# Optimization experiments

Measured on AMD Instinct MI355X. Metric: run time of the kernel, lower is better.

Reference implementation:

```python
import jax, jax.numpy as jnp
import numpy as np

MESH_SIZE = 0.01
HIDDEN = 256
NUM_LAYERS = 3
TEMP = 1e-3          # soft-relay temperature (forward default)
H_SCALE = 0.0        # soft-magnet: mu0*H << B
M_SCALE = 0.5
M_OFFSET = 0.5


def _make_mesh():
    # Uniform triangular Preisach mesh: points (beta, alpha) with 0 <= beta <= alpha <= 1.
    k = int(round(1.0 / MESH_SIZE)) + 1  # 101 grid lines -> 5151 points
    g = np.linspace(0.0, 1.0, k, dtype=np.float32)
    bb, aa = np.meshgrid(g, g, indexing='ij')
    sel = bb <= aa
    return jnp.asarray(np.stack([bb[sel], aa[sel]], axis=-1))  # [N, 2] = (beta, alpha)


def setup_inputs() -> dict:
    key = jax.random.key(0)
    ks = jax.random.split(key, 10)
    mesh = _make_mesh()                       # [N, 2]
    n = mesh.shape[0]
    B, CTXT, T = 8, 128, 2048
    encoder_input = jax.random.uniform(ks[0], (B, CTXT, 2), dtype=jnp.float32)
    decoder_input = jax.random.uniform(ks[1], (B, T, 1), dtype=jnp.float32)
    initial_states = 2.0 * jax.random.uniform(ks[2], (B, n), dtype=jnp.float32) - 1.0  # s in [-1, 1]
    y0 = jax.random.uniform(ks[3], (B,), dtype=jnp.float32)
    # ResNetMLP density network params (input_dim=2, output_dim=1)
    W_in = jax.random.normal(ks[4], (2, HIDDEN), dtype=jnp.float32) * 0.5
    b_in = jnp.zeros((HIDDEN,), dtype=jnp.float32)
    W_blk = jax.random.normal(ks[5], (NUM_LAYERS, HIDDEN, HIDDEN), dtype=jnp.float32) * (1.0 / np.sqrt(HIDDEN))
    b_blk = jnp.zeros((NUM_LAYERS, HIDDEN), dtype=jnp.float32)
    W_out = jax.random.normal(ks[6], (HIDDEN, 1), dtype=jnp.float32) * (1.0 / np.sqrt(HIDDEN))
    b_out = jnp.zeros((1,), dtype=jnp.float32)
    return {'encoder_input': encoder_input, 'decoder_input': decoder_input,
            'initial_states': initial_states, 'y0': y0, 'mesh': mesh,
            'W_in': W_in, 'b_in': b_in, 'W_blk': W_blk, 'b_blk': b_blk,
            'W_out': W_out, 'b_out': b_out}


def _density(mesh, W_in, b_in, W_blk, b_blk, W_out, b_out):
    # ResNetMLP (eval: dropout off) + sigmoid (normalized_density=True)
    h = jax.nn.relu(mesh @ W_in + b_in)
    for i in range(NUM_LAYERS):  # small fixed layer loop
        h = h + jax.nn.relu(h @ W_blk[i] + b_blk[i])
    return jax.nn.sigmoid((h @ W_out + b_out)[..., 0])  # [N]


def _get_states(h_seq, alpha, beta, s0, h0):
    # Sequential soft-relay hysteron update across time.
    # h_seq [B,T], alpha/beta [N], s0 [B,N], h0 [B]
    def step(carry, h_t):  # h_t [B]
        s, h_prev = carry
        up = jax.nn.sigmoid((h_t[:, None] - alpha[None, :]) / TEMP)   # switch to +1 when h > alpha
        dn = jax.nn.sigmoid((h_t[:, None] - beta[None, :]) / TEMP)    # stay/unswitch vs beta when sweeping down
        s_up = s + (1.0 - s) * up            # increasing field branch
        s_dn = -1.0 + (s + 1.0) * dn         # decreasing field branch
        inc = (h_t >= h_prev)[:, None]
        s_new = jnp.where(inc, s_up, s_dn)
        return (s_new, h_t), s_new
    (_, _), states = jax.lax.scan(step, (s0, h0), jnp.swapaxes(h_seq, 0, 1))
    return jnp.swapaxes(states, 0, 1)  # [B, T, N]


def reference(encoder_input, decoder_input, initial_states, y0, mesh,
              W_in, b_in, W_blk, b_blk, W_out, b_out):
    B = encoder_input.shape[0]
    n = mesh.shape[0]
    beta = mesh[:, 0]
    alpha = mesh[:, 1]
    density = _density(mesh, W_in, b_in, W_blk, b_blk, W_out, b_out)  # [N] (shared mesh, eval)
    h = decoder_input[..., 0]                                          # [B, T]
    states = _get_states(h, alpha, beta, initial_states, y0)           # [B, T, N]
    m = jnp.einsum('n,btn->bt', density, states) / jnp.sum(density)    # [B, T]
    b_norm = H_SCALE * h + M_SCALE * m + M_OFFSET
    density_b = jnp.broadcast_to(density, (B, n))
    mesh_b = jnp.broadcast_to(mesh, (B,) + mesh.shape)
    return (b_norm, density_b, m, initial_states, mesh_b)
```

## Files before the change

kernel.cpp:

```cpp
#include <hip/hip_runtime.h>
#include <hip/hip_fp16.h>
#include <math.h>

#define N_MESH   5151
#define NB       8
#define TT       2048
#define HID      256
#define NLAYERS  3
#define NCHUNK   64
#define CHUNK    32
#define NG       101
#define TROW     40
#define NQ       11
#define NPAD     5632
#define SCAN_GRID 512
#define PREP_NBLK 48
#define COPY_NBLK 61
#define MLP_NBLK  81
#define PH2_NBLK  88
#define DENSB_NBLK 21

#define OFF_SGV   144
#define OFF_TAB   272
#define SMEM1     8352
#define OFF_RED   8352
#define OFF_DRED  12960
#define SMEM3     13088

#define WS_DENSITY 0
#define WS_WT      6144
#define WS_PQ      104448

#define OUT_BNORM  0
#define OUT_DENSB  16384
#define OUT_M      57592
#define OUT_S0     73976
#define OUT_MESHB  115184

typedef _Float16 half8  __attribute__((ext_vector_type(8)));
typedef unsigned short u16x8 __attribute__((ext_vector_type(8)));
typedef float    f32x4  __attribute__((ext_vector_type(4)));

__device__ __forceinline__ float sigmoid_fast(float x) {
    float e = __expf(-x);
    return __builtin_amdgcn_rcpf(1.0f + e);
}

__device__ __forceinline__ int swz(int row, int kbyte) {
    return row * 512 + (kbyte ^ ((row & 7) << 4));
}

__device__ __forceinline__ float dpp16_sum(float v) {
    int a;
    a = __builtin_amdgcn_update_dpp(0, __float_as_int(v), 0xB1, 0xF, 0xF, true);
    v += __int_as_float(a);
    a = __builtin_amdgcn_update_dpp(0, __float_as_int(v), 0x4E, 0xF, 0xF, true);
    v += __int_as_float(a);
    a = __builtin_amdgcn_update_dpp(0, __float_as_int(v), 0x141, 0xF, 0xF, true);
    v += __int_as_float(a);
    a = __builtin_amdgcn_update_dpp(0, __float_as_int(v), 0x140, 0xF, 0xF, true);
    v += __int_as_float(a);
    return v;
}

__device__ __forceinline__ void build_table(int tid, const float* hs2,
                                            float* sgv, unsigned short* tab)
{
    if (tid < CHUNK) sgv[tid] = (hs2[tid + 1] >= hs2[tid]) ? 1.0f : -1.0f;
    for (int idx = tid; idx < NG * CHUNK; idx += 512) {
        int g = idx >> 5;
        int t = idx & 31;
        float ht = hs2[t + 1];
        bool inc = (ht >= hs2[t]);
        float bx = ht * 1000.0f;
        float y = inc ? fmaf(-10.f, (float)g, bx) : fmaf(10.f, (float)g, -bx);
        float A = __builtin_amdgcn_rcpf(1.0f + __expf(y));
        tab[g * TROW + t] = __half_as_ushort(__float2half(A));
    }
}

template<int Q0, int GS>
__device__ __forceinline__ void grp_pr(const unsigned short* tab,
    const int (&ga)[NQ], const int (&gb)[NQ], float (&P)[NQ], float (&R)[NQ],
    const float (&sg8)[8], float gstart, int tb)
{
    u16x8 ra[GS], rb[GS];
#pragma unroll
    for (int q = 0; q < GS; ++q) {
        ra[q] = *(const u16x8*)&tab[ga[Q0 + q] * TROW + tb];
        rb[q] = *(const u16x8*)&tab[gb[Q0 + q] * TROW + tb];
    }
    float gp = gstart;
#pragma unroll
    for (int j = 0; j < 8; ++j) {
        float sgt = sg8[j];
        float dl = gp - sgt;
        gp = sgt;
        bool inc = sgt > 0.0f;
#pragma unroll
        for (int q = 0; q < GS; ++q) {
            unsigned short u = inc ? ra[q][j] : rb[q][j];
            float A = __half2float(__ushort_as_half(u));
            float r = R[Q0 + q] + dl;
            P[Q0 + q] *= A;
            R[Q0 + q] = r * A;
        }
    }
}

template<int Q0, int GS>
__device__ __forceinline__ void grp_z(const unsigned short* tab,
    const int (&ga)[NQ], const int (&gb)[NQ], float (&z)[NQ],
    const float (&d)[NQ], const float (&sg8)[8], float (&v)[8],
    float gstart, int tb)
{
    u16x8 ra[GS], rb[GS];
#pragma unroll
    for (int q = 0; q < GS; ++q) {
        ra[q] = *(const u16x8*)&tab[ga[Q0 + q] * TROW + tb];
        rb[q] = *(const u16x8*)&tab[gb[Q0 + q] * TROW + tb];
    }
    float gp = gstart;
#pragma unroll
    for (int j = 0; j < 8; ++j) {
        float sgt = sg8[j];
        float dl = gp - sgt;
        gp = sgt;
        bool inc = sgt > 0.0f;
        float a = 0.f;
#pragma unroll
        for (int q = 0; q < GS; ++q) {
            unsigned short u = inc ? ra[q][j] : rb[q][j];
            float A = __half2float(__ushort_as_half(u));
            float zn = (z[Q0 + q] + dl) * A;
            z[Q0 + q] = zn;
            a = fmaf(d[Q0 + q], zn, a);
        }
        v[j] += a;
    }
}

__global__ __launch_bounds__(512, 4) void k1_scan1_prep(
    const float* __restrict__ dec, const float* __restrict__ y0,
    const float* __restrict__ mesh, const float* __restrict__ Wblk,
    float2* __restrict__ PQ, half8* __restrict__ WT,
    const float* __restrict__ s0, float* __restrict__ out)
{
    __shared__ __align__(16) char smem[SMEM1];
    const int tid = threadIdx.x;
    const int bid = blockIdx.x;

    if (bid >= SCAN_GRID + PREP_NBLK) {
        int idx = bid - (SCAN_GRID + PREP_NBLK);
        const int n1 = NB * N_MESH;
        const int total = 3 * n1;
#pragma unroll
        for (int k = 0; k < 4; ++k) {
            int j = idx * 2048 + k * 512 + tid;
            if (j < total) {
                if (j < n1) out[OUT_S0 + j] = s0[j];
                else {
                    int jj = j - n1;
                    out[OUT_MESHB + jj] = mesh[jj % (2 * N_MESH)];
                }
            }
        }
        return;
    }

    if (bid >= SCAN_GRID) {
        int g = (bid - SCAN_GRID) * 512 + tid;
        int l  = g & 63;
        int nt = (g >> 6) & 15;
        int kg = (g >> 10) & 7;
        int L  = g >> 13;
        int n  = nt * 16 + (l & 15);
        int kb = kg * 32 + ((l >> 4) & 3) * 8;
        const float* Wb = Wblk + (size_t)L * HID * HID;
        half8 v;
#pragma unroll
        for (int i = 0; i < 8; ++i)
            v[i] = (_Float16)Wb[(size_t)(kb + i) * HID + n];
        WT[g] = v;
        return;
    }

    float* hs2 = (float*)smem;
    float* sgv = (float*)(smem + OFF_SGV);
    unsigned short* tab = (unsigned short*)(smem + OFF_TAB);

    const int b = bid & 7;
    const int c = bid >> 3;
    const int t0 = c * CHUNK;

    if (tid < CHUNK) hs2[tid + 1] = dec[b * TT + t0 + tid];
    if (tid == 0) hs2[0] = (c == 0) ? y0[b] : dec[b * TT + t0 - 1];

    int ga[NQ], gb[NQ];
#pragma unroll
    for (int q = 0; q < NQ; ++q) {
        int n = q * 512 + tid;
        if (n < N_MESH) {
            gb[q] = (int)(mesh[2 * n]     * 100.0f + 0.5f);
            ga[q] = (int)(mesh[2 * n + 1] * 100.0f + 0.5f);
        } else { ga[q] = 0; gb[q] = 0; }
    }
    __syncthreads();
    build_table(tid, hs2, sgv, tab);
    __syncthreads();

    float P[NQ], R[NQ];
    float gprev = sgv[0];
#pragma unroll
    for (int q = 0; q < NQ; ++q) { P[q] = 1.f; R[q] = -gprev; }

    for (int tb = 0; tb < CHUNK; tb += 8) {
        float4 sA = *(const float4*)&sgv[tb];
        float4 sB = *(const float4*)&sgv[tb + 4];
        float sg8[8] = {sA.x, sA.y, sA.z, sA.w, sB.x, sB.y, sB.z, sB.w};
        float gs = gprev;
        grp_pr<0, 4>(tab, ga, gb, P, R, sg8, gs, tb);
        grp_pr<4, 4>(tab, ga, gb, P, R, sg8, gs, tb);
        grp_pr<8, 3>(tab, ga, gb, P, R, sg8, gs, tb);
        gprev = sg8[7];
    }
    size_t basew = ((size_t)(c * NB + b)) * NPAD;
#pragma unroll
    for (int q = 0; q < NQ; ++q) {
        float2 v; v.x = P[q]; v.y = R[q] + gprev;
        PQ[basew + q * 512 + tid] = v;
    }
}

__global__ __launch_bounds__(512) void k2_mlp_phase2(
    const float* __restrict__ mesh, const float* __restrict__ Win,
    const float* __restrict__ bin,  const half8* __restrict__ WT,
    const float* __restrict__ bblk, const float* __restrict__ Wout,
    const float* __restrict__ bout, float* __restrict__ density,
    const float* __restrict__ s0_in, float* __restrict__ PQf)
{
    __shared__ __align__(16) char hA[64 * 512];
    __shared__ float psum[4][16][2];
    const int tid  = threadIdx.x;

    if (blockIdx.x >= MLP_NBLK) {
        int idx = blockIdx.x - MLP_NBLK;
        int nbb = idx % NQ;
        int b   = idx / NQ;
        int n   = nbb * 512 + tid;
        const float2* PQ = (const float2*)PQf;
        float s = (n < N_MESH) ? s0_in[b * N_MESH + n] : 0.f;
#pragma unroll 4
        for (int c = 0; c < NCHUNK; ++c) {
            size_t ix = ((size_t)(c * NB + b)) * NPAD + n;
            float2 pv = PQ[ix];
            PQf[2 * ix] = s;
            s = fmaf(pv.x, s, pv.y);
        }
        return;
    }

    const int w    = tid >> 6;
    const int lane = tid & 63;
    const int rl   = lane & 15;
    const int cg   = lane >> 4;
    const int mt   = w & 3;
    const int nh   = w >> 2;
    const int row0 = blockIdx.x * 64;

    float hreg[8][4];

    {
        float m0[4], m1[4];
#pragma unroll
        for (int r = 0; r < 4; ++r) {
            int gr = row0 + mt * 16 + cg * 4 + r;
            if (gr < N_MESH) { m0[r] = mesh[2 * gr]; m1[r] = mesh[2 * gr + 1]; }
            else { m0[r] = 0.f; m1[r] = 0.f; }
        }
#pragma unroll
        for (int j = 0; j < 8; ++j) {
            int col = nh * 128 + j * 16 + rl;
            float wa = Win[col], wb = Win[HID + col], bi = bin[col];
#pragma unroll
            for (int r = 0; r < 4; ++r) {
                float v = fmaxf(fmaf(m0[r], wa, fmaf(m1[r], wb, bi)), 0.f);
                hreg[j][r] = v;
                *(_Float16*)(hA + swz(mt * 16 + cg * 4 + r, col * 2)) =
                    (_Float16)v;
            }
        }
    }
    __syncthreads();

    for (int L = 0; L < NLAYERS; ++L) {
        half8 af[8];
#pragma unroll
        for (int kg = 0; kg < 8; ++kg)
            af[kg] = *(const half8*)(hA + swz(mt * 16 + rl, kg * 64 + cg * 16));
        __syncthreads();

        float bias[8];
#pragma unroll
        for (int j = 0; j < 8; ++j)
            bias[j] = bblk[L * HID + nh * 128 + j * 16 + rl];

        f32x4 acc[8];
#pragma unroll
        for (int j = 0; j < 8; ++j) acc[j] = (f32x4){0.f, 0.f, 0.f, 0.f};

        const half8* WTL = WT + ((size_t)(L * 8) * 16 + nh * 8) * 64 + lane;
        half8 b0[8], b1[8];
#pragma unroll
        for (int j = 0; j < 8; ++j) b0[j] = WTL[(size_t)j * 64];
#pragma unroll
        for (int kg2 = 0; kg2 < 8; kg2 += 2) {
#pragma unroll
            for (int j = 0; j < 8; ++j)
                b1[j] = WTL[(size_t)(kg2 + 1) * 1024 + (size_t)j * 64];
#pragma unroll
            for (int j = 0; j < 8; ++j)
                acc[j] = __builtin_amdgcn_mfma_f32_16x16x32_f16(
                    af[kg2], b0[j], acc[j], 0, 0, 0);
            if (kg2 + 2 < 8) {
#pragma unroll
                for (int j = 0; j < 8; ++j)
                    b0[j] = WTL[(size_t)(kg2 + 2) * 1024 + (size_t)j * 64];
            }
#pragma unroll
            for (int j = 0; j < 8; ++j)
                acc[j] = __builtin_amdgcn_mfma_f32_16x16x32_f16(
                    af[kg2 + 1], b1[j], acc[j], 0, 0, 0);
        }

#pragma unroll
        for (int j = 0; j < 8; ++j) {
            int col = nh * 128 + j * 16 + rl;
#pragma unroll
            for (int r = 0; r < 4; ++r) {
                float v = hreg[j][r] + fmaxf(acc[j][r] + bias[j], 0.f);
                hreg[j][r] = v;
                if (L < NLAYERS - 1)
                    *(_Float16*)(hA + swz(mt * 16 + cg * 4 + r, col * 2)) =
                        (_Float16)v;
            }
        }
        if (L < NLAYERS - 1) __syncthreads();
    }

    {
        float p[4] = {0.f, 0.f, 0.f, 0.f};
#pragma unroll
        for (int j = 0; j < 8; ++j) {
            float wo = Wout[nh * 128 + j * 16 + rl];
#pragma unroll
            for (int r = 0; r < 4; ++r) p[r] = fmaf(hreg[j][r], wo, p[r]);
        }
#pragma unroll
        for (int st = 1; st < 16; st <<= 1)
#pragma unroll
            for (int r = 0; r < 4; ++r) p[r] += __shfl_xor(p[r], st, 64);
        if (rl == 0) {
#pragma unroll
            for (int r = 0; r < 4; ++r) psum[mt][cg * 4 + r][nh] = p[r];
        }
    }
    __syncthreads();
    if (tid < 64) {
        int gr = row0 + tid;
        float pp = psum[tid >> 4][tid & 15][0] + psum[tid >> 4][tid & 15][1];
        if (gr < N_MESH) density[gr] = sigmoid_fast(pp + bout[0]);
    }
}

__global__ __launch_bounds__(512, 4) void k3_phase3_fin(
    const float* __restrict__ dec, const float* __restrict__ y0,
    const float* __restrict__ mesh, const float* __restrict__ density,
    const float* __restrict__ PQf, float* __restrict__ out)
{
    __shared__ __align__(16) char smem[SMEM3];
    const int tid = threadIdx.x;
    const int bid = blockIdx.x;

    if (bid >= SCAN_GRID) {
        int idx = bid - SCAN_GRID;
#pragma unroll
        for (int k = 0; k < 4; ++k) {
            int j = idx * 2048 + k * 512 + tid;
            if (j < NB * N_MESH) out[OUT_DENSB + j] = density[j % N_MESH];
        }
        return;
    }

    float* hs2 = (float*)smem;
    float* sgv = (float*)(smem + OFF_SGV);
    unsigned short* tab = (unsigned short*)(smem + OFF_TAB);
    float* red  = (float*)(smem + OFF_RED);
    float* Dred = (float*)(smem + OFF_DRED);

    const int b = bid & 7;
    const int c = bid >> 3;
    const int t0 = c * CHUNK;

    if (tid < CHUNK) hs2[tid + 1] = dec[b * TT + t0 + tid];
    if (tid == 0) hs2[0] = (c == 0) ? y0[b] : dec[b * TT + t0 - 1];

    int ga[NQ], gb[NQ];
    float d[NQ], S[NQ];
#pragma unroll
    for (int q = 0; q < NQ; ++q) {
        int n = q * 512 + tid;
        if (n < N_MESH) {
            gb[q] = (int)(mesh[2 * n]     * 100.0f + 0.5f);
            ga[q] = (int)(mesh[2 * n + 1] * 100.0f + 0.5f);
            d[q]  = density[n];
            S[q]  = PQf[2 * (((size_t)(c * NB + b)) * NPAD + n)];
        } else { ga[q] = 0; gb[q] = 0; d[q] = 0.f; S[q] = 0.f; }
    }
    {
        float Dp = 0.f;
#pragma unroll
        for (int q = 0; q < NQ; ++q) Dp += d[q];
        Dp = dpp16_sum(Dp);
        if ((tid & 15) == 0) Dred[tid >> 4] = Dp;
    }
    __syncthreads();
    build_table(tid, hs2, sgv, tab);
    __syncthreads();

    float z[NQ];
    float gprev = sgv[0];
#pragma unroll
    for (int q = 0; q < NQ; ++q) z[q] = S[q] - gprev;

    for (int tb = 0; tb < CHUNK; tb += 8) {
        float4 sA = *(const float4*)&sgv[tb];
        float4 sB = *(const float4*)&sgv[tb + 4];
        float sg8[8] = {sA.x, sA.y, sA.z, sA.w, sB.x, sB.y, sB.z, sB.w};
        float v[8] = {0.f, 0.f, 0.f, 0.f, 0.f, 0.f, 0.f, 0.f};
        float gs = gprev;
        grp_z<0, 4>(tab, ga, gb, z, d, sg8, v, gs, tb);
        grp_z<4, 4>(tab, ga, gb, z, d, sg8, v, gs, tb);
        grp_z<8, 3>(tab, ga, gb, z, d, sg8, v, gs, tb);
        gprev = sg8[7];

#pragma unroll
        for (int j = 0; j < 8; ++j) v[j] = dpp16_sum(v[j]);
        float outv = v[0];
#pragma unroll
        for (int j = 1; j < 8; ++j) if ((tid & 15) == j) outv = v[j];
        if ((tid & 15) < 8)
            red[(tb + (tid & 15)) * 36 + (tid >> 4)] = outv;
    }
    __syncthreads();

    if (tid < CHUNK) {
        float acc = 0.f;
#pragma unroll
        for (int g4 = 0; g4 < 32; g4 += 4) {
            float4 r4 = *(const float4*)&red[tid * 36 + g4];
            acc += (r4.x + r4.y) + (r4.z + r4.w);
        }
        float D = 0.f;
#pragma unroll
        for (int g4 = 0; g4 < 32; g4 += 4) {
            float4 d4 = *(const float4*)&Dred[g4];
            D += (d4.x + d4.y) + (d4.z + d4.w);
        }
        float gd = sgv[tid];
        int t = t0 + tid;
        float m = (acc + gd * D) / D;
        out[OUT_M + b * TT + t] = m;
        out[OUT_BNORM + b * TT + t] = 0.5f * m + 0.5f;
    }
}

extern "C" void kernel_launch(void* const* d_in, const int* in_sizes, int n_in,
                              void* d_out, int out_size, void* d_ws, size_t ws_size,
                              hipStream_t stream) {
    const float* dec  = (const float*)d_in[1];
    const float* s0   = (const float*)d_in[2];
    const float* y0   = (const float*)d_in[3];
    const float* mesh = (const float*)d_in[4];
    const float* Win  = (const float*)d_in[5];
    const float* bin  = (const float*)d_in[6];
    const float* Wblk = (const float*)d_in[7];
    const float* bblk = (const float*)d_in[8];
    const float* Wout = (const float*)d_in[9];
    const float* bout = (const float*)d_in[10];
    float* out = (float*)d_out;
    float* ws  = (float*)d_ws;

    float*  density  = ws + WS_DENSITY;
    half8*  wt       = (half8*)(ws + WS_WT);
    float*  pqf      = ws + WS_PQ;
    float2* pq       = (float2*)pqf;

    k1_scan1_prep<<<SCAN_GRID + PREP_NBLK + COPY_NBLK, 512, 0, stream>>>(
        dec, y0, mesh, Wblk, pq, wt, s0, out);
    k2_mlp_phase2<<<MLP_NBLK + PH2_NBLK, 512, 0, stream>>>(
        mesh, Win, bin, wt, bblk, Wout, bout, density, s0, pqf);
    k3_phase3_fin<<<SCAN_GRID + DENSB_NBLK, 512, 0, stream>>>(
        dec, y0, mesh, density, pqf, out);
}
```

Baseline: 74.06 us.

## Replace per-gridline sigmoid LDS table with closed-form clamped linear relay factor

Drops the per-chunk 101x32 half-precision sigmoid table and its gathered LDS loads. At TEMP=1e-3 the sigmoid is treated as saturating within one grid step, so each relay factor becomes a clamped linear function of the grid index: fmed3(sign*g + c, 0, 1). The offset c is set from a single sigmoid evaluated at the nearest grid line per timestep. This removes the table build and per-element gathers, cuts shared memory, and uses only a few ALU ops per element. It depends on the narrow sigmoid width relative to mesh spacing, so it is exact only for this temperature and mesh.

```diff
diff --git a/kernel.cpp b/kernel.cpp
--- a/kernel.cpp
+++ b/kernel.cpp
@@ -9,8 +9,6 @@
 #define NLAYERS  3
 #define NCHUNK   64
 #define CHUNK    32
-#define NG       101
-#define TROW     40
 #define NQ       11
 #define NPAD     5632
 #define SCAN_GRID 512
@@ -20,12 +18,11 @@
 #define PH2_NBLK  88
 #define DENSB_NBLK 21
 
-#define OFF_SGV   144
-#define OFF_TAB   272
-#define SMEM1     8352
-#define OFF_RED   8352
-#define OFF_DRED  12960
-#define SMEM3     13088
+#define OFF_TP    144
+#define SMEM1     656
+#define OFF_RED   656
+#define OFF_DRED  5264
+#define SMEM3     5392
 
 #define WS_DENSITY 0
 #define WS_WT      6144
@@ -38,7 +35,6 @@
 #define OUT_MESHB  115184
 
 typedef _Float16 half8  __attribute__((ext_vector_type(8)));
-typedef unsigned short u16x8 __attribute__((ext_vector_type(8)));
 typedef float    f32x4  __attribute__((ext_vector_type(4)));
 
 __device__ __forceinline__ float sigmoid_fast(float x) {
@@ -63,80 +59,29 @@
     return v;
 }
 
-__device__ __forceinline__ void build_table(int tid, const float* hs2,
-                                            float* sgv, unsigned short* tab)
+__device__ __forceinline__ void build_params(int tid, const float* hs2,
+                                             float4* tp)
 {
-    if (tid < CHUNK) sgv[tid] = (hs2[tid + 1] >= hs2[tid]) ? 1.0f : -1.0f;
-    for (int idx = tid; idx < NG * CHUNK; idx += 512) {
-        int g = idx >> 5;
-        int t = idx & 31;
-        float ht = hs2[t + 1];
-        bool inc = (ht >= hs2[t]);
-        float bx = ht * 1000.0f;
-        float y = inc ? fmaf(-10.f, (float)g, bx) : fmaf(10.f, (float)g, -bx);
-        float A = __builtin_amdgcn_rcpf(1.0f + __expf(y));
-        tab[g * TROW + t] = __half_as_ushort(__float2half(A));
-    }
-}
-
-template<int Q0, int GS>
-__device__ __forceinline__ void grp_pr(const unsigned short* tab,
-    const int (&ga)[NQ], const int (&gb)[NQ], float (&P)[NQ], float (&R)[NQ],
-    const float (&sg8)[8], float gstart, int tb)
-{
-    u16x8 ra[GS], rb[GS];
-#pragma unroll
-    for (int q = 0; q < GS; ++q) {
-        ra[q] = *(const u16x8*)&tab[ga[Q0 + q] * TROW + tb];
-        rb[q] = *(const u16x8*)&tab[gb[Q0 + q] * TROW + tb];
-    }
-    float gp = gstart;
-#pragma unroll
-    for (int j = 0; j < 8; ++j) {
-        float sgt = sg8[j];
-        float dl = gp - sgt;
-        gp = sgt;
-        bool inc = sgt > 0.0f;
-#pragma unroll
-        for (int q = 0; q < GS; ++q) {
-            unsigned short u = inc ? ra[q][j] : rb[q][j];
-            float A = __half2float(__ushort_as_half(u));
-            float r = R[Q0 + q] + dl;
-            P[Q0 + q] *= A;
-            R[Q0 + q] = r * A;
-        }
-    }
-}
-
-template<int Q0, int GS>
-__device__ __forceinline__ void grp_z(const unsigned short* tab,
-    const int (&ga)[NQ], const int (&gb)[NQ], float (&z)[NQ],
-    const float (&d)[NQ], const float (&sg8)[8], float (&v)[8],
-    float gstart, int tb)
-{
-    u16x8 ra[GS], rb[GS];
-#pragma unroll
-    for (int q = 0; q < GS; ++q) {
-        ra[q] = *(const u16x8*)&tab[ga[Q0 + q] * TROW + tb];
-        rb[q] = *(const u16x8*)&tab[gb[Q0 + q] * TROW + tb];
-    }
-    float gp = gstart;
-#pragma unroll
-    for (int j = 0; j < 8; ++j) {
-        float sgt = sg8[j];
-        float dl = gp - sgt;
-        gp = sgt;
-        bool inc = sgt > 0.0f;
-        float a = 0.f;
-#pragma unroll
-        for (int q = 0; q < GS; ++q) {
-            unsigned short u = inc ? ra[q][j] : rb[q][j];
-            float A = __half2float(__ushort_as_half(u));
-            float zn = (z[Q0 + q] + dl) * A;
-            z[Q0 + q] = zn;
-            a = fmaf(d[Q0 + q], zn, a);
-        }
-        v[j] += a;
+    if (tid < CHUNK) {
+        float ht = hs2[tid + 1];
+        float hp = hs2[tid];
+        bool inc = (ht >= hp);
+        float sg = inc ? 1.f : -1.f;
+        float psg = sg;
+        if (tid > 0) psg = (hs2[tid] >= hs2[tid - 1]) ? 1.f : -1.f;
+        float x = ht * 1000.f;
+        float gc = rintf(ht * 100.f);
+        float4 p;
+        p.x = psg - sg;
+        if (inc) {
+            float Ac = sigmoid_fast(fmaf(10.f, gc, -x));
+            p.y = 1.f;  p.z = Ac - gc;
+        } else {
+            float Ac = sigmoid_fast(fmaf(-10.f, gc, x));
+            p.y = -1.f; p.z = gc + Ac;
+        }
+        p.w = sg;
+        tp[tid] = p;
     }
 }
 
@@ -186,8 +131,7 @@
     }
 
     float* hs2 = (float*)smem;
-    float* sgv = (float*)(smem + OFF_SGV);
-    unsigned short* tab = (unsigned short*)(smem + OFF_TAB);
+    float4* tp = (float4*)(smem + OFF_TP);
 
     const int b = bid & 7;
     const int c = bid >> 3;
@@ -196,38 +140,44 @@
     if (tid < CHUNK) hs2[tid + 1] = dec[b * TT + t0 + tid];
     if (tid == 0) hs2[0] = (c == 0) ? y0[b] : dec[b * TT + t0 - 1];
 
-    int ga[NQ], gb[NQ];
+    float fga[NQ], fgb[NQ];
 #pragma unroll
     for (int q = 0; q < NQ; ++q) {
         int n = q * 512 + tid;
         if (n < N_MESH) {
-            gb[q] = (int)(mesh[2 * n]     * 100.0f + 0.5f);
-            ga[q] = (int)(mesh[2 * n + 1] * 100.0f + 0.5f);
-        } else { ga[q] = 0; gb[q] = 0; }
-    }
-    __syncthreads();
-    build_table(tid, hs2, sgv, tab);
+            fgb[q] = rintf(mesh[2 * n]     * 100.0f);
+            fga[q] = rintf(mesh[2 * n + 1] * 100.0f);
+        } else { fga[q] = 0.f; fgb[q] = 0.f; }
+    }
+    __syncthreads();
+    build_params(tid, hs2, tp);
     __syncthreads();
 
     float P[NQ], R[NQ];
-    float gprev = sgv[0];
-#pragma unroll
-    for (int q = 0; q < NQ; ++q) { P[q] = 1.f; R[q] = -gprev; }
+    float sg0 = tp[0].w;
+#pragma unroll
+    for (int q = 0; q < NQ; ++q) { P[q] = 1.f; R[q] = -sg0; }
 
     for (int tb = 0; tb < CHUNK; tb += 8) {
-        float4 sA = *(const float4*)&sgv[tb];
-        float4 sB = *(const float4*)&sgv[tb + 4];
-        float sg8[8] = {sA.x, sA.y, sA.z, sA.w, sB.x, sB.y, sB.z, sB.w};
-        float gs = gprev;
-        grp_pr<0, 4>(tab, ga, gb, P, R, sg8, gs, tb);
-        grp_pr<4, 4>(tab, ga, gb, P, R, sg8, gs, tb);
-        grp_pr<8, 3>(tab, ga, gb, P, R, sg8, gs, tb);
-        gprev = sg8[7];
-    }
+#pragma unroll
+        for (int j = 0; j < 8; ++j) {
+            float4 p = tp[tb + j];
+            bool inc = p.y > 0.f;
+#pragma unroll
+            for (int q = 0; q < NQ; ++q) {
+                float gq = inc ? fga[q] : fgb[q];
+                float A = __builtin_amdgcn_fmed3f(fmaf(p.y, gq, p.z), 0.f, 1.f);
+                float r = R[q] + p.x;
+                P[q] *= A;
+                R[q] = r * A;
+            }
+        }
+    }
+    float sgl = tp[CHUNK - 1].w;
     size_t basew = ((size_t)(c * NB + b)) * NPAD;
 #pragma unroll
     for (int q = 0; q < NQ; ++q) {
-        float2 v; v.x = P[q]; v.y = R[q] + gprev;
+        float2 v; v.x = P[q]; v.y = R[q] + sgl;
         PQ[basew + q * 512 + tid] = v;
     }
 }
@@ -393,8 +343,7 @@
     }
 
     float* hs2 = (float*)smem;
-    float* sgv = (float*)(smem + OFF_SGV);
-    unsigned short* tab = (unsigned short*)(smem + OFF_TAB);
+    float4* tp = (float4*)(smem + OFF_TP);
     float* red  = (float*)(smem + OFF_RED);
     float* Dred = (float*)(smem + OFF_DRED);
 
@@ -405,17 +354,17 @@
     if (tid < CHUNK) hs2[tid + 1] = dec[b * TT + t0 + tid];
     if (tid == 0) hs2[0] = (c == 0) ? y0[b] : dec[b * TT + t0 - 1];
 
-    int ga[NQ], gb[NQ];
+    float fga[NQ], fgb[NQ];
     float d[NQ], S[NQ];
 #pragma unroll
     for (int q = 0; q < NQ; ++q) {
         int n = q * 512 + tid;
         if (n < N_MESH) {
-            gb[q] = (int)(mesh[2 * n]     * 100.0f + 0.5f);
-            ga[q] = (int)(mesh[2 * n + 1] * 100.0f + 0.5f);
+            fgb[q] = rintf(mesh[2 * n]     * 100.0f);
+            fga[q] = rintf(mesh[2 * n + 1] * 100.0f);
             d[q]  = density[n];
             S[q]  = PQf[2 * (((size_t)(c * NB + b)) * NPAD + n)];
-        } else { ga[q] = 0; gb[q] = 0; d[q] = 0.f; S[q] = 0.f; }
+        } else { fga[q] = 0.f; fgb[q] = 0.f; d[q] = 0.f; S[q] = 0.f; }
     }
     {
         float Dp = 0.f;
@@ -425,25 +374,32 @@
         if ((tid & 15) == 0) Dred[tid >> 4] = Dp;
     }
     __syncthreads();
-    build_table(tid, hs2, sgv, tab);
+    build_params(tid, hs2, tp);
     __syncthreads();
 
     float z[NQ];
-    float gprev = sgv[0];
-#pragma unroll
-    for (int q = 0; q < NQ; ++q) z[q] = S[q] - gprev;
+    float sg0 = tp[0].w;
+#pragma unroll
+    for (int q = 0; q < NQ; ++q) z[q] = S[q] - sg0;
 
     for (int tb = 0; tb < CHUNK; tb += 8) {
-        float4 sA = *(const float4*)&sgv[tb];
-        float4 sB = *(const float4*)&sgv[tb + 4];
-        float sg8[8] = {sA.x, sA.y, sA.z, sA.w, sB.x, sB.y, sB.z, sB.w};
-        float v[8] = {0.f, 0.f, 0.f, 0.f, 0.f, 0.f, 0.f, 0.f};
-        float gs = gprev;
-        grp_z<0, 4>(tab, ga, gb, z, d, sg8, v, gs, tb);
-        grp_z<4, 4>(tab, ga, gb, z, d, sg8, v, gs, tb);
-        grp_z<8, 3>(tab, ga, gb, z, d, sg8, v, gs, tb);
-        gprev = sg8[7];
-
+        float v[8];
+#pragma unroll
+        for (int j = 0; j < 8; ++j) {
+            float4 p = tp[tb + j];
+            bool inc = p.y > 0.f;
+            float a0 = 0.f, a1 = 0.f;
+#pragma unroll
+            for (int q = 0; q < NQ; ++q) {
+                float gq = inc ? fga[q] : fgb[q];
+                float A = __builtin_amdgcn_fmed3f(fmaf(p.y, gq, p.z), 0.f, 1.f);
+                float zn = (z[q] + p.x) * A;
+                z[q] = zn;
+                if (q & 1) a1 = fmaf(d[q], zn, a1);
+                else       a0 = fmaf(d[q], zn, a0);
+            }
+            v[j] = a0 + a1;
+        }
 #pragma unroll
         for (int j = 0; j < 8; ++j) v[j] = dpp16_sum(v[j]);
         float outv = v[0];
@@ -467,7 +423,7 @@
             float4 d4 = *(const float4*)&Dred[g4];
             D += (d4.x + d4.y) + (d4.z + d4.w);
         }
-        float gd = sgv[tid];
+        float gd = tp[tid].w;
         int t = t0 + tid;
         float m = (acc + gd * D) / D;
         out[OUT_M + b * TT + t] = m;
```

New measurement: 67.07 us. -9.4%, faster.
